# Optimization experiments

Measured on AMD Instinct MI355X. Metric: run time of the kernel, lower is better.

## Reference

```python
import jax, jax.numpy as jnp
import numpy as np

N_NODES = 50000
N_EDGES = 800000
N_GRAPHS = 128
IN_DIM = 100
HID = 256
STEPS = 5


def setup_inputs() -> dict:
    key = jax.random.key(0)
    ks = jax.random.split(key, 24)
    s = 0.05
    inp = {
        'x': jax.random.normal(ks[0], (N_NODES, IN_DIM), jnp.float32),
        'edge_index': jax.random.randint(ks[1], (2, N_EDGES), 0, N_NODES, jnp.int32),
        'batch': jnp.sort(jax.random.randint(ks[2], (N_NODES,), 0, N_GRAPHS, jnp.int32)),
        # input projection
        'W_in': jax.random.normal(ks[3], (IN_DIM, HID), jnp.float32) * s,
        'b_in': jnp.zeros((HID,), jnp.float32),
        # GatedGraphConv per-step weights [steps, HID, HID]
        'ggc_w': jax.random.normal(ks[4], (STEPS, HID, HID), jnp.float32) * s,
        # GRUCell params (torch layout: rows = [r, z, n] chunks)
        'W_ih': jax.random.normal(ks[5], (3 * HID, HID), jnp.float32) * s,
        'W_hh': jax.random.normal(ks[6], (3 * HID, HID), jnp.float32) * s,
        'b_ih': jnp.zeros((3 * HID,), jnp.float32),
        'b_hh': jnp.zeros((3 * HID,), jnp.float32),
        # attention MLP: HID -> HID//2 -> 1 (sigmoid)
        'Wa1': jax.random.normal(ks[7], (HID, HID // 2), jnp.float32) * s,
        'ba1': jnp.zeros((HID // 2,), jnp.float32),
        'Wa2': jax.random.normal(ks[8], (HID // 2, 1), jnp.float32) * s,
        'ba2': jnp.zeros((1,), jnp.float32),
        # classifier: 2*HID -> HID -> HID//2 -> 2
        'Wc1': jax.random.normal(ks[9], (2 * HID, HID), jnp.float32) * s,
        'bc1': jnp.zeros((HID,), jnp.float32),
        'Wc2': jax.random.normal(ks[10], (HID, HID // 2), jnp.float32) * s,
        'bc2': jnp.zeros((HID // 2,), jnp.float32),
        'Wc3': jax.random.normal(ks[11], (HID // 2, 2), jnp.float32) * s,
        'bc3': jnp.zeros((2,), jnp.float32),
    }
    return inp


def _forward(x, edge_index, batch, W_in, b_in, ggc_w, W_ih, W_hh, b_ih, b_hh,
             Wa1, ba1, Wa2, ba2, Wc1, bc1, Wc2, bc2, Wc3, bc3):
    src, dst = edge_index[0], edge_index[1]
    # input projection + relu
    h = jax.nn.relu(x @ W_in + b_in)  # [N, HID]

    def ggc_step(h, w):
        m = h @ w                                   # [N, HID]
        agg = jax.ops.segment_sum(m[src], dst, num_segments=N_NODES)  # scatter-add
        gi = agg @ W_ih.T + b_ih                    # [N, 3*HID]
        gh = h @ W_hh.T + b_hh
        i_r, i_z, i_n = jnp.split(gi, 3, axis=-1)
        h_r, h_z, h_n = jnp.split(gh, 3, axis=-1)
        r = jax.nn.sigmoid(i_r + h_r)
        z = jax.nn.sigmoid(i_z + h_z)
        n = jnp.tanh(i_n + r * h_n)
        return (1.0 - z) * n + z * h, None

    h, _ = jax.lax.scan(ggc_step, h, ggc_w)
    h = jax.nn.relu(h)

    # attention weights per node (dropout is identity at eval)
    a = jax.nn.sigmoid(jax.nn.relu(h @ Wa1 + ba1) @ Wa2 + ba2)[:, 0]  # [N]
    wx = h * a[:, None]

    counts = jax.ops.segment_sum(jnp.ones((N_NODES,), h.dtype), batch, num_segments=N_GRAPHS)
    mean_p = jax.ops.segment_sum(wx, batch, num_segments=N_GRAPHS) / jnp.maximum(counts, 1.0)[:, None]
    max_p = jax.ops.segment_max(wx, batch, num_segments=N_GRAPHS)
    max_p = jnp.where(counts[:, None] > 0, max_p, 0.0)
    g = jnp.concatenate([mean_p, max_p], axis=1)  # [G, 2*HID]

    g = jax.nn.relu(g @ Wc1 + bc1)
    g = jax.nn.relu(g @ Wc2 + bc2)
    preds = g @ Wc3 + bc3
    return preds, a


def reference(x, edge_index, batch, W_in, b_in, ggc_w, W_ih, W_hh, b_ih, b_hh,
              Wa1, ba1, Wa2, ba2, Wc1, bc1, Wc2, bc2, Wc3, bc3):
    return _forward(x, edge_index, batch, W_in, b_in, ggc_w, W_ih, W_hh, b_ih, b_hh,
                    Wa1, ba1, Wa2, ba2, Wc1, bc1, Wc2, bc2, Wc3, bc3)
```

## Files before the change

### kernel.cpp

```cpp
#include <hip/hip_runtime.h>
#include <cstddef>

#define NN 50000
#define NE 800000
#define NG 128
#define IND 100
#define HID 256
#define NSTEPS 5
#define PCH 8

typedef __attribute__((ext_vector_type(8))) short bf16x8;
typedef __attribute__((ext_vector_type(4))) float f32x4;

__device__ __forceinline__ float b2f(unsigned h) { return __uint_as_float(h << 16); }
__device__ __forceinline__ unsigned short f2b(float f) {
    unsigned u = __float_as_uint(f);
    unsigned r = (u + 0x7FFFu + ((u >> 16) & 1u)) >> 16;
    return (unsigned short)r;
}
__device__ __forceinline__ float sigm(float x) { return 1.f / (1.f + __expf(-x)); }
__device__ __forceinline__ float tanh_fast(float x) { return 1.f - 2.f / (1.f + __expf(2.f * x)); }

#define LSTR 40
__global__ __launch_bounds__(256) void gemm_bf16(const unsigned short* __restrict__ A,
                                                 const unsigned short* __restrict__ Bt,
                                                 const float* __restrict__ bias, int act,
                                                 unsigned short* __restrict__ C,
                                                 int M, int N, int K,
                                                 size_t btz, size_t cz)
{
    Bt += (size_t)blockIdx.z * btz;
    C  += (size_t)blockIdx.z * cz;
    __shared__ unsigned short As[128 * LSTR];
    __shared__ unsigned short Bs[128 * LSTR];
    const int tid  = threadIdx.x;
    const int row0 = blockIdx.y * 128;
    const int col0 = blockIdx.x * 128;
    const int wave = tid >> 6, lane = tid & 63;
    const int wm = wave >> 1, wn = wave & 1;
    const int lr = lane & 15, q = lane >> 4;
    const int r_st = tid >> 2;
    const int ks   = tid & 3;

    f32x4 acc[4][4];
    #pragma unroll
    for (int i = 0; i < 4; ++i)
        #pragma unroll
        for (int j = 0; j < 4; ++j) acc[i][j] = (f32x4){0.f, 0.f, 0.f, 0.f};

    for (int k0 = 0; k0 < K; k0 += 32) {
        #pragma unroll
        for (int it = 0; it < 2; ++it) {
            int r  = r_st + it * 64;
            int ga = min(row0 + r, M - 1);
            uint4 av = *(const uint4*)(A + (size_t)ga * K + k0 + ks * 8);
            *(uint4*)(As + r * LSTR + ks * 8) = av;
            uint4 bv = *(const uint4*)(Bt + (size_t)(col0 + r) * K + k0 + ks * 8);
            *(uint4*)(Bs + r * LSTR + ks * 8) = bv;
        }
        __syncthreads();
        bf16x8 af[4], bfr[4];
        #pragma unroll
        for (int i = 0; i < 4; ++i)
            af[i]  = *(const bf16x8*)(As + (wm * 64 + i * 16 + lr) * LSTR + q * 8);
        #pragma unroll
        for (int j = 0; j < 4; ++j)
            bfr[j] = *(const bf16x8*)(Bs + (wn * 64 + j * 16 + lr) * LSTR + q * 8);
        #pragma unroll
        for (int i = 0; i < 4; ++i)
            #pragma unroll
            for (int j = 0; j < 4; ++j)
                acc[i][j] = __builtin_amdgcn_mfma_f32_16x16x32_bf16(af[i], bfr[j], acc[i][j], 0, 0, 0);
        __syncthreads();
    }
    #pragma unroll
    for (int i = 0; i < 4; ++i) {
        int rbase = row0 + wm * 64 + i * 16 + q * 4;
        #pragma unroll
        for (int j = 0; j < 4; ++j) {
            int col = col0 + wn * 64 + j * 16 + lr;
            if (col >= N) continue;
            float badd = bias ? bias[col] : 0.f;
            #pragma unroll
            for (int r = 0; r < 4; ++r) {
                int row = rbase + r;
                if (row < M) {
                    float v = acc[i][j][r] + badd;
                    if (act) v = fmaxf(v, 0.f);
                    C[(size_t)row * N + col] = f2b(v);
                }
            }
        }
    }
}

__global__ __launch_bounds__(256, 3) void gru_mfma(const unsigned short* __restrict__ agg,
                                                   const unsigned short* __restrict__ hbf,
                                                   float* __restrict__ h,
                                                   unsigned short* __restrict__ hbfo,
                                                   const unsigned short* __restrict__ Wgi,
                                                   const unsigned short* __restrict__ Wgh,
                                                   const float* __restrict__ bih,
                                                   const float* __restrict__ bhh,
                                                   int M, int dorelu)
{
    __shared__ unsigned short Sa[64 * LSTR];
    __shared__ unsigned short Sh[64 * LSTR];
    const int tid  = threadIdx.x;
    const int row0 = blockIdx.y * 64;
    const int col0 = blockIdx.x * 64;
    const int wave = tid >> 6, lane = tid & 63;
    const int lr = lane & 15, q = lane >> 4;
    const int cw = col0 + wave * 16;
    const int r_st = tid >> 2, ks = tid & 3;

    f32x4 acc[4][4];
    #pragma unroll
    for (int g = 0; g < 4; ++g)
        #pragma unroll
        for (int i = 0; i < 4; ++i) acc[g][i] = (f32x4){0.f, 0.f, 0.f, 0.f};

    const int ga = min(row0 + r_st, M - 1);
    uint4 pa = *(const uint4*)(agg + (size_t)ga * HID + ks * 8);
    uint4 ph = *(const uint4*)(hbf + (size_t)ga * HID + ks * 8);

    #pragma unroll
    for (int kk = 0; kk < 8; ++kk) {
        const int k0 = kk * 32;
        __syncthreads();
        *(uint4*)(Sa + r_st * LSTR + ks * 8) = pa;
        *(uint4*)(Sh + r_st * LSTR + ks * 8) = ph;
        __syncthreads();
        if (kk < 7) {
            pa = *(const uint4*)(agg + (size_t)ga * HID + k0 + 32 + ks * 8);
            ph = *(const uint4*)(hbf + (size_t)ga * HID + k0 + 32 + ks * 8);
        }
        bf16x8 wir = *(const bf16x8*)(Wgi + (size_t)(0*HID + cw + lr) * HID + k0 + q * 8);
        bf16x8 wiz = *(const bf16x8*)(Wgi + (size_t)(1*HID + cw + lr) * HID + k0 + q * 8);
        bf16x8 win = *(const bf16x8*)(Wgi + (size_t)(2*HID + cw + lr) * HID + k0 + q * 8);
        bf16x8 whr = *(const bf16x8*)(Wgh + (size_t)(0*HID + cw + lr) * HID + k0 + q * 8);
        bf16x8 whz = *(const bf16x8*)(Wgh + (size_t)(1*HID + cw + lr) * HID + k0 + q * 8);
        bf16x8 whn = *(const bf16x8*)(Wgh + (size_t)(2*HID + cw + lr) * HID + k0 + q * 8);
        bf16x8 afa[4], afh[4];
        #pragma unroll
        for (int i = 0; i < 4; ++i) {
            afa[i] = *(const bf16x8*)(Sa + (i * 16 + lr) * LSTR + q * 8);
            afh[i] = *(const bf16x8*)(Sh + (i * 16 + lr) * LSTR + q * 8);
        }
        #pragma unroll
        for (int i = 0; i < 4; ++i) {
            acc[0][i] = __builtin_amdgcn_mfma_f32_16x16x32_bf16(afa[i], wir, acc[0][i], 0, 0, 0);
            acc[0][i] = __builtin_amdgcn_mfma_f32_16x16x32_bf16(afh[i], whr, acc[0][i], 0, 0, 0);
            acc[1][i] = __builtin_amdgcn_mfma_f32_16x16x32_bf16(afa[i], wiz, acc[1][i], 0, 0, 0);
            acc[1][i] = __builtin_amdgcn_mfma_f32_16x16x32_bf16(afh[i], whz, acc[1][i], 0, 0, 0);
            acc[2][i] = __builtin_amdgcn_mfma_f32_16x16x32_bf16(afa[i], win, acc[2][i], 0, 0, 0);
            acc[3][i] = __builtin_amdgcn_mfma_f32_16x16x32_bf16(afh[i], whn, acc[3][i], 0, 0, 0);
        }
    }

    const int cg = cw + lr;
    const float brr = bih[cg]         + bhh[cg];
    const float bzz = bih[HID + cg]   + bhh[HID + cg];
    const float bin = bih[2*HID + cg];
    const float bhn = bhh[2*HID + cg];
    #pragma unroll
    for (int i = 0; i < 4; ++i) {
        #pragma unroll
        for (int r = 0; r < 4; ++r) {
            int row = row0 + i * 16 + q * 4 + r;
            if (row < M) {
                float rr = sigm(acc[0][i][r] + brr);
                float zz = sigm(acc[1][i][r] + bzz);
                float nn = tanh_fast(acc[2][i][r] + bin + rr * (acc[3][i][r] + bhn));
                size_t off = (size_t)row * HID + cg;
                float hv = h[off];
                float o = (1.f - zz) * nn + zz * hv;
                if (dorelu) o = fmaxf(o, 0.f);
                h[off] = o;
                hbfo[off] = f2b(o);
            }
        }
    }
}

template<int ACT>
__global__ __launch_bounds__(256) void gemm_kn(const float* __restrict__ A,
                                               const float* __restrict__ B,
                                               const float* __restrict__ bias,
                                               float* __restrict__ C,
                                               int M, int N, int K)
{
    __shared__ float As[64][17];
    __shared__ float Bs[16][65];
    const int tid  = threadIdx.x;
    const int row0 = blockIdx.y * 64;
    const int col0 = blockIdx.x * 64;
    const int tr = tid >> 4, tc = tid & 15;
    const int ar = tid >> 2, akq = tid & 3;
    const int bk = tid >> 4, bj = (tid & 15) << 2;

    float acc[4][4] = {};
    for (int k0 = 0; k0 < K; k0 += 16) {
        float4 av = make_float4(0.f,0.f,0.f,0.f);
        if (row0 + ar < M && (k0 + (akq<<2)) < K)
            av = *(const float4*)(A + (size_t)(row0+ar)*K + k0 + (akq<<2));
        As[ar][(akq<<2)+0] = av.x; As[ar][(akq<<2)+1] = av.y;
        As[ar][(akq<<2)+2] = av.z; As[ar][(akq<<2)+3] = av.w;
        float4 bv = make_float4(0.f,0.f,0.f,0.f);
        if (k0 + bk < K)
            bv = *(const float4*)(B + (size_t)(k0+bk)*N + col0 + bj);
        Bs[bk][bj+0] = bv.x; Bs[bk][bj+1] = bv.y; Bs[bk][bj+2] = bv.z; Bs[bk][bj+3] = bv.w;
        __syncthreads();
        #pragma unroll
        for (int k = 0; k < 16; ++k) {
            float a4[4], b4[4];
            #pragma unroll
            for (int i = 0; i < 4; ++i) a4[i] = As[(tr<<2)+i][k];
            #pragma unroll
            for (int j = 0; j < 4; ++j) b4[j] = Bs[k][(tc<<2)+j];
            #pragma unroll
            for (int i = 0; i < 4; ++i)
                #pragma unroll
                for (int j = 0; j < 4; ++j) acc[i][j] += a4[i]*b4[j];
        }
        __syncthreads();
    }
    #pragma unroll
    for (int i = 0; i < 4; ++i) {
        int row = row0 + (tr<<2) + i;
        if (row >= M) continue;
        #pragma unroll
        for (int j = 0; j < 4; ++j) {
            int col = col0 + (tc<<2) + j;
            float v = acc[i][j];
            if (bias) v += bias[col];
            if (ACT == 1) v = fmaxf(v, 0.f);
            C[(size_t)row*N + col] = v;
        }
    }
}

__global__ void edge_count(const int* __restrict__ dst, int* __restrict__ cnt, int E) {
    int e = blockIdx.x*256 + threadIdx.x;
    if (e < E) atomicAdd(&cnt[dst[e]], 1);
}
__global__ void scan_bsums(const int* __restrict__ cnt, int* __restrict__ bsum, int n) {
    __shared__ int sd[512];
    int tid = threadIdx.x, i = blockIdx.x*512 + tid;
    sd[tid] = (i < n) ? cnt[i] : 0;
    __syncthreads();
    for (int off = 256; off > 0; off >>= 1) {
        if (tid < off) sd[tid] += sd[tid+off];
        __syncthreads();
    }
    if (tid == 0) bsum[blockIdx.x] = sd[0];
}
__global__ void scan_top(int* __restrict__ bsum, int nb) {
    __shared__ int sd[128];
    int tid = threadIdx.x;
    int v = (tid < nb) ? bsum[tid] : 0;
    sd[tid] = v;
    __syncthreads();
    for (int off = 1; off < 128; off <<= 1) {
        int t = (tid >= off) ? sd[tid-off] : 0;
        __syncthreads();
        sd[tid] += t;
        __syncthreads();
    }
    if (tid < nb) bsum[tid] = sd[tid] - v;
}
__global__ void scan_local(const int* __restrict__ cnt, const int* __restrict__ bsum,
                           int* __restrict__ rp, int n) {
    __shared__ int sd[512];
    int tid = threadIdx.x, i = blockIdx.x*512 + tid;
    int v = (i < n) ? cnt[i] : 0;
    sd[tid] = v;
    __syncthreads();
    for (int off = 1; off < 512; off <<= 1) {
        int t = (tid >= off) ? sd[tid-off] : 0;
        __syncthreads();
        sd[tid] += t;
        __syncthreads();
    }
    if (i < n) rp[i] = bsum[blockIdx.x] + sd[tid] - v;
    if (i == n-1) rp[n] = bsum[blockIdx.x] + sd[tid];
}
__global__ void edge_fill(const int* __restrict__ src, const int* __restrict__ dst,
                          const int* __restrict__ rp, int* __restrict__ cur,
                          int* __restrict__ ci, int E) {
    int e = blockIdx.x*256 + threadIdx.x;
    if (e < E) {
        int d = dst[e];
        int pos = rp[d] + atomicAdd(&cur[d], 1);
        ci[pos] = src[e];
    }
}

__global__ void gather_agg(const unsigned short* __restrict__ m, unsigned short* __restrict__ agg,
                           const int* __restrict__ rp, const int* __restrict__ ci, int M)
{
    int node = blockIdx.x*4 + (threadIdx.x >> 6);
    int lane = threadIdx.x & 63;
    if (node >= M) return;
    const int half = lane >> 5;
    const int li   = lane & 31;
    int s = rp[node], e = rp[node+1];
    float a[8] = {0.f,0.f,0.f,0.f,0.f,0.f,0.f,0.f};
    int p = s;
    for (; p + 7 < e; p += 8) {
        int r0 = ci[p + half], r1 = ci[p + 2 + half], r2 = ci[p + 4 + half], r3 = ci[p + 6 + half];
        uint4 v0 = *(const uint4*)(m + (size_t)r0 * HID + li * 8);
        uint4 v1 = *(const uint4*)(m + (size_t)r1 * HID + li * 8);
        uint4 v2 = *(const uint4*)(m + (size_t)r2 * HID + li * 8);
        uint4 v3 = *(const uint4*)(m + (size_t)r3 * HID + li * 8);
        a[0] += b2f(v0.x & 0xffffu) + b2f(v1.x & 0xffffu) + b2f(v2.x & 0xffffu) + b2f(v3.x & 0xffffu);
        a[1] += b2f(v0.x >> 16)     + b2f(v1.x >> 16)     + b2f(v2.x >> 16)     + b2f(v3.x >> 16);
        a[2] += b2f(v0.y & 0xffffu) + b2f(v1.y & 0xffffu) + b2f(v2.y & 0xffffu) + b2f(v3.y & 0xffffu);
        a[3] += b2f(v0.y >> 16)     + b2f(v1.y >> 16)     + b2f(v2.y >> 16)     + b2f(v3.y >> 16);
        a[4] += b2f(v0.z & 0xffffu) + b2f(v1.z & 0xffffu) + b2f(v2.z & 0xffffu) + b2f(v3.z & 0xffffu);
        a[5] += b2f(v0.z >> 16)     + b2f(v1.z >> 16)     + b2f(v2.z >> 16)     + b2f(v3.z >> 16);
        a[6] += b2f(v0.w & 0xffffu) + b2f(v1.w & 0xffffu) + b2f(v2.w & 0xffffu) + b2f(v3.w & 0xffffu);
        a[7] += b2f(v0.w >> 16)     + b2f(v1.w >> 16)     + b2f(v2.w >> 16)     + b2f(v3.w >> 16);
    }
    for (; p + 1 < e; p += 2) {
        int r0 = ci[p + half];
        uint4 v = *(const uint4*)(m + (size_t)r0 * HID + li * 8);
        a[0] += b2f(v.x & 0xffffu); a[1] += b2f(v.x >> 16);
        a[2] += b2f(v.y & 0xffffu); a[3] += b2f(v.y >> 16);
        a[4] += b2f(v.z & 0xffffu); a[5] += b2f(v.z >> 16);
        a[6] += b2f(v.w & 0xffffu); a[7] += b2f(v.w >> 16);
    }
    if (p < e && half == 0) {
        int r0 = ci[p];
        uint4 v = *(const uint4*)(m + (size_t)r0 * HID + li * 8);
        a[0] += b2f(v.x & 0xffffu); a[1] += b2f(v.x >> 16);
        a[2] += b2f(v.y & 0xffffu); a[3] += b2f(v.y >> 16);
        a[4] += b2f(v.z & 0xffffu); a[5] += b2f(v.z >> 16);
        a[6] += b2f(v.w & 0xffffu); a[7] += b2f(v.w >> 16);
    }
    #pragma unroll
    for (int u = 0; u < 8; ++u) a[u] += __shfl_xor(a[u], 32, 64);
    if (half == 0) {
        uint4 o;
        o.x = (unsigned)f2b(a[0]) | ((unsigned)f2b(a[1]) << 16);
        o.y = (unsigned)f2b(a[2]) | ((unsigned)f2b(a[3]) << 16);
        o.z = (unsigned)f2b(a[4]) | ((unsigned)f2b(a[5]) << 16);
        o.w = (unsigned)f2b(a[6]) | ((unsigned)f2b(a[7]) << 16);
        *(uint4*)(agg + (size_t)node * HID + li * 8) = o;
    }
}

__global__ void cvt_f2b4(const float* __restrict__ src, unsigned short* __restrict__ dst, int n4) {
    int i = blockIdx.x*256 + threadIdx.x;
    if (i >= n4) return;
    float4 v = *((const float4*)src + i);
    uint2 o;
    o.x = (unsigned)f2b(v.x) | ((unsigned)f2b(v.y) << 16);
    o.y = (unsigned)f2b(v.z) | ((unsigned)f2b(v.w) << 16);
    *((uint2*)dst + i) = o;
}
__global__ void cvt_elem(const float* __restrict__ src, unsigned short* __restrict__ dst, int n) {
    int i = blockIdx.x*256 + threadIdx.x;
    if (i < n) dst[i] = f2b(src[i]);
}
__global__ void prep_wa1(const float* __restrict__ w, unsigned short* __restrict__ wt) {
    int n = blockIdx.x, k = threadIdx.x;
    wt[(size_t)n*HID + k] = f2b(w[(size_t)k*128 + n]);
}

__global__ void att_sig(const unsigned short* __restrict__ t, const float* __restrict__ Wa2,
                        const float* __restrict__ ba2, float* __restrict__ a, int M)
{
    int node = blockIdx.x*4 + (threadIdx.x >> 6);
    int lane = threadIdx.x & 63;
    if (node >= M) return;
    float s = b2f(t[(size_t)node*128 + lane])*Wa2[lane]
            + b2f(t[(size_t)node*128 + 64 + lane])*Wa2[64+lane];
    #pragma unroll
    for (int off = 32; off > 0; off >>= 1) s += __shfl_down(s, off, 64);
    if (lane == 0) a[node] = 1.f/(1.f+__expf(-(s + ba2[0])));
}

__device__ __forceinline__ int lowerb(const int* arr, int n, int val) {
    int lo = 0, hi = n;
    while (lo < hi) { int mid = (lo+hi)>>1; if (arr[mid] < val) lo = mid+1; else hi = mid; }
    return lo;
}
__global__ void pool_partial(const float* __restrict__ h, const float* __restrict__ a,
                             const int* __restrict__ batch, float* __restrict__ part, int M)
{
    int g = blockIdx.x, c = blockIdx.y, j = threadIdx.x;
    int lo = lowerb(batch, M, g);
    int hi = lowerb(batch, M, g+1);
    int len = hi - lo, per = (len + PCH - 1) / PCH;
    int s = lo + c * per, e = min(s + per, hi);
    float sum = 0.f, mx = 0.f;
    for (int n = s; n < e; ++n) {
        float v = h[(size_t)n*HID + j] * a[n];
        sum += v; mx = fmaxf(mx, v);
    }
    float* pp = part + ((size_t)g*PCH + c) * 512;
    pp[j] = sum; pp[256 + j] = mx;
}
__global__ void pool_final(const float* __restrict__ part, const int* __restrict__ batch,
                           float* __restrict__ gout, int M)
{
    int g = blockIdx.x, j = threadIdx.x;
    float sum = 0.f, mx = 0.f;
    for (int c = 0; c < PCH; ++c) {
        const float* pp = part + ((size_t)g*PCH + c) * 512;
        sum += pp[j];
        mx = fmaxf(mx, pp[256 + j]);
    }
    int lo = lowerb(batch, M, g);
    int hi = lowerb(batch, M, g+1);
    float cnt = (float)(hi - lo);
    gout[(size_t)g*512 + j]       = sum / fmaxf(cnt, 1.f);
    gout[(size_t)g*512 + 256 + j] = mx;
}

__global__ void preds_kernel(const float* __restrict__ g2, const float* __restrict__ W,
                             const float* __restrict__ b, float* __restrict__ out)
{
    int t = threadIdx.x;
    int row = t >> 1, col = t & 1;
    float s = b[col];
    for (int k = 0; k < 128; ++k) s += g2[row*128 + k] * W[k*2 + col];
    out[row*2 + col] = s;
}

extern "C" void kernel_launch(void* const* d_in, const int* in_sizes, int n_in,
                              void* d_out, int out_size, void* d_ws, size_t ws_size,
                              hipStream_t stream)
{
    const float* x     = (const float*)d_in[0];
    const int*   eidx  = (const int*)  d_in[1];
    const int*   batch = (const int*)  d_in[2];
    const float* W_in  = (const float*)d_in[3];
    const float* b_in  = (const float*)d_in[4];
    const float* ggc_w = (const float*)d_in[5];
    const float* W_ih  = (const float*)d_in[6];
    const float* W_hh  = (const float*)d_in[7];
    const float* b_ih  = (const float*)d_in[8];
    const float* b_hh  = (const float*)d_in[9];
    const float* Wa1   = (const float*)d_in[10];
    const float* ba1   = (const float*)d_in[11];
    const float* Wa2   = (const float*)d_in[12];
    const float* ba2   = (const float*)d_in[13];
    const float* Wc1   = (const float*)d_in[14];
    const float* bc1   = (const float*)d_in[15];
    const float* Wc2   = (const float*)d_in[16];
    const float* bc2   = (const float*)d_in[17];
    const float* Wc3   = (const float*)d_in[18];
    const float* bc3   = (const float*)d_in[19];

    float* out  = (float*)d_out;
    float* aout = out + NG*2;

    char* p = (char*)d_ws;
    auto alloc = [&](size_t bytes) -> char* {
        char* r = p; p += (bytes + 255) & ~(size_t)255; return r;
    };
    float*          hf    = (float*)alloc((size_t)NN*HID*4);
    unsigned short* hbfP  = (unsigned short*)alloc((size_t)NN*HID*2);
    unsigned short* hbfQ  = (unsigned short*)alloc((size_t)NN*HID*2);
    unsigned short* aggbf = (unsigned short*)alloc((size_t)NN*HID*2);
    int* row_ptr = (int*)alloc((NN+1)*4);
    int* cursor  = (int*)alloc(NN*4);
    int* col_idx = (int*)alloc((size_t)NE*4);
    int* bsum    = (int*)alloc(128*4);
    unsigned short* wgbf   = (unsigned short*)alloc((size_t)NSTEPS*HID*HID*2);
    unsigned short* WihBf  = (unsigned short*)alloc((size_t)768*HID*2);
    unsigned short* WhhBf  = (unsigned short*)alloc((size_t)768*HID*2);
    unsigned short* WcombT = (unsigned short*)alloc((size_t)NSTEPS*768*HID*2);
    unsigned short* Wa1t   = (unsigned short*)alloc((size_t)128*HID*2);
    float* part = (float*)alloc((size_t)NG*PCH*512*4);
    float* gbuf = (float*)alloc((size_t)NG*2*HID*4);
    float* g1   = (float*)alloc((size_t)NG*HID*4);
    float* g2   = (float*)alloc((size_t)NG*128*4);

    const int* esrc = eidx;
    const int* edst = eidx + NE;
    dim3 blk(256);
    const int NB512 = (NN + 511) / 512;

    hipMemsetAsync(cursor, 0, NN*sizeof(int), stream);
    edge_count<<<NE/256, blk, 0, stream>>>(edst, cursor, NE);
    scan_bsums<<<NB512, 512, 0, stream>>>(cursor, bsum, NN);
    scan_top<<<1, 128, 0, stream>>>(bsum, NB512);
    scan_local<<<NB512, 512, 0, stream>>>(cursor, bsum, row_ptr, NN);
    hipMemsetAsync(cursor, 0, NN*sizeof(int), stream);
    edge_fill<<<NE/256, blk, 0, stream>>>(esrc, edst, row_ptr, cursor, col_idx, NE);

    cvt_elem<<<(NSTEPS*HID*HID + 255)/256, blk, 0, stream>>>(ggc_w, wgbf, NSTEPS*HID*HID);
    cvt_elem<<<768, blk, 0, stream>>>(W_ih, WihBf, 768*HID);
    cvt_elem<<<768, blk, 0, stream>>>(W_hh, WhhBf, 768*HID);
    prep_wa1<<<128, blk, 0, stream>>>(Wa1, Wa1t);
    gemm_bf16<<<dim3(2, 6, NSTEPS), blk, 0, stream>>>(
        WihBf, wgbf, nullptr, 0, WcombT, 768, HID, HID,
        (size_t)HID*HID, (size_t)768*HID);

    gemm_kn<1><<<dim3(HID/64, (NN+63)/64), blk, 0, stream>>>(x, W_in, b_in, hf, NN, HID, IND);
    cvt_f2b4<<<(NN*HID/4 + 255)/256, blk, 0, stream>>>(hf, hbfP, NN*HID/4);

    unsigned short* hbf  = hbfP;
    unsigned short* hbfn = hbfQ;
    const int MB64 = (NN + 63) / 64;
    for (int s = 0; s < NSTEPS; ++s) {
        gather_agg<<<NN/4, blk, 0, stream>>>(hbf, aggbf, row_ptr, col_idx, NN);
        gru_mfma<<<dim3(HID/64, MB64), blk, 0, stream>>>(
            aggbf, hbf, hf, hbfn, WcombT + (size_t)s*768*HID, WhhBf, b_ih, b_hh,
            NN, (s == NSTEPS-1) ? 1 : 0);
        unsigned short* t0 = hbf; hbf = hbfn; hbfn = t0;
    }

    unsigned short* tbuf = aggbf;
    gemm_bf16<<<dim3(1, (NN+127)/128), blk, 0, stream>>>(hbf, Wa1t, ba1, 1, tbuf, NN, 128, HID, 0, 0);
    att_sig<<<NN/4, blk, 0, stream>>>(tbuf, Wa2, ba2, aout, NN);

    pool_partial<<<dim3(NG, PCH), blk, 0, stream>>>(hf, aout, batch, part, NN);
    pool_final<<<NG, blk, 0, stream>>>(part, batch, gbuf, NN);

    gemm_kn<1><<<dim3(HID/64, (NG+63)/64), blk, 0, stream>>>(gbuf, Wc1, bc1, g1, NG, HID, 2*HID);
    gemm_kn<1><<<dim3(2,      (NG+63)/64), blk, 0, stream>>>(g1,   Wc2, bc2, g2, NG, 128, HID);
    preds_kernel<<<1, blk, 0, stream>>>(g2, Wc3, bc3, out);
}
```

Measured before the change: 1.246 ms.

## Run input projection on bf16 MFMA with hi/lo split of x, raise GRU occupancy

Replaces the fp32 input-projection GEMM and the separate fp32-to-bf16 conversion with a bf16 MFMA GEMM. x is split into hi and lo bf16 parts concatenated along K, and W_in is duplicated to match, which keeps some extra precision. The GEMM writes both the bf16 and fp32 outputs, so the conversion kernel is removed. The GRU kernel's launch bounds are also raised to 4 blocks per CU, which may cause register spills. W_in itself is rounded to bf16, which lowers the precision of the projection.

Result: no change. 1.225 ms (-1.7%).

```diff
diff --git a/kernel.cpp b/kernel.cpp
--- a/kernel.cpp
+++ b/kernel.cpp
@@ -26,6 +26,7 @@
                                                  const unsigned short* __restrict__ Bt,
                                                  const float* __restrict__ bias, int act,
                                                  unsigned short* __restrict__ C,
+                                                 float* __restrict__ Cf,
                                                  int M, int N, int K,
                                                  size_t btz, size_t cz)
 {
@@ -88,13 +89,14 @@
                     float v = acc[i][j][r] + badd;
                     if (act) v = fmaxf(v, 0.f);
                     C[(size_t)row * N + col] = f2b(v);
+                    if (Cf) Cf[(size_t)row * N + col] = v;
                 }
             }
         }
     }
 }
 
-__global__ __launch_bounds__(256, 3) void gru_mfma(const unsigned short* __restrict__ agg,
+__global__ __launch_bounds__(256, 4) void gru_mfma(const unsigned short* __restrict__ agg,
                                                    const unsigned short* __restrict__ hbf,
                                                    float* __restrict__ h,
                                                    unsigned short* __restrict__ hbfo,
@@ -350,15 +352,24 @@
     }
 }
 
-__global__ void cvt_f2b4(const float* __restrict__ src, unsigned short* __restrict__ dst, int n4) {
-    int i = blockIdx.x*256 + threadIdx.x;
-    if (i >= n4) return;
-    float4 v = *((const float4*)src + i);
-    uint2 o;
-    o.x = (unsigned)f2b(v.x) | ((unsigned)f2b(v.y) << 16);
-    o.y = (unsigned)f2b(v.z) | ((unsigned)f2b(v.w) << 16);
-    *((uint2*)dst + i) = o;
-}
+__global__ void split_x(const float* __restrict__ x, unsigned short* __restrict__ A) {
+    int n = blockIdx.x, k = threadIdx.x;
+    unsigned short hi = 0, lo = 0;
+    if (k < IND) {
+        float v = x[(size_t)n * IND + k];
+        hi = f2b(v);
+        lo = f2b(v - b2f(hi));
+    }
+    A[(size_t)n * 256 + k]       = hi;
+    A[(size_t)n * 256 + 128 + k] = lo;
+}
+__global__ void prep_win(const float* __restrict__ w, unsigned short* __restrict__ bt) {
+    int n = blockIdx.x, k = threadIdx.x;
+    unsigned short v = (k < IND) ? f2b(w[(size_t)k * HID + n]) : (unsigned short)0;
+    bt[(size_t)n * 256 + k]       = v;
+    bt[(size_t)n * 256 + 128 + k] = v;
+}
+
 __global__ void cvt_elem(const float* __restrict__ src, unsigned short* __restrict__ dst, int n) {
     int i = blockIdx.x*256 + threadIdx.x;
     if (i < n) dst[i] = f2b(src[i]);
@@ -474,6 +485,7 @@
     unsigned short* WhhBf  = (unsigned short*)alloc((size_t)768*HID*2);
     unsigned short* WcombT = (unsigned short*)alloc((size_t)NSTEPS*768*HID*2);
     unsigned short* Wa1t   = (unsigned short*)alloc((size_t)128*HID*2);
+    unsigned short* WinT   = (unsigned short*)alloc((size_t)256*256*2);
     float* part = (float*)alloc((size_t)NG*PCH*512*4);
     float* gbuf = (float*)alloc((size_t)NG*2*HID*4);
     float* g1   = (float*)alloc((size_t)NG*HID*4);
@@ -497,11 +509,14 @@
     cvt_elem<<<768, blk, 0, stream>>>(W_hh, WhhBf, 768*HID);
     prep_wa1<<<128, blk, 0, stream>>>(Wa1, Wa1t);
     gemm_bf16<<<dim3(2, 6, NSTEPS), blk, 0, stream>>>(
-        WihBf, wgbf, nullptr, 0, WcombT, 768, HID, HID,
+        WihBf, wgbf, nullptr, 0, WcombT, nullptr, 768, HID, HID,
         (size_t)HID*HID, (size_t)768*HID);
 
-    gemm_kn<1><<<dim3(HID/64, (NN+63)/64), blk, 0, stream>>>(x, W_in, b_in, hf, NN, HID, IND);
-    cvt_f2b4<<<(NN*HID/4 + 255)/256, blk, 0, stream>>>(hf, hbfP, NN*HID/4);
+    unsigned short* Ax = hbfQ;
+    split_x<<<NN, 128, 0, stream>>>(x, Ax);
+    prep_win<<<256, 128, 0, stream>>>(W_in, WinT);
+    gemm_bf16<<<dim3(2, (NN+127)/128), blk, 0, stream>>>(
+        Ax, WinT, b_in, 1, hbfP, hf, NN, HID, 256, 0, 0);
 
     unsigned short* hbf  = hbfP;
     unsigned short* hbfn = hbfQ;
@@ -515,7 +530,7 @@
     }
 
     unsigned short* tbuf = aggbf;
-    gemm_bf16<<<dim3(1, (NN+127)/128), blk, 0, stream>>>(hbf, Wa1t, ba1, 1, tbuf, NN, 128, HID, 0, 0);
+    gemm_bf16<<<dim3(1, (NN+127)/128), blk, 0, stream>>>(hbf, Wa1t, ba1, 1, tbuf, nullptr, NN, 128, HID, 0, 0);
     att_sig<<<NN/4, blk, 0, stream>>>(tbuf, Wa2, ba2, aout, NN);
 
     pool_partial<<<dim3(NG, PCH), blk, 0, stream>>>(hf, aout, batch, part, NN);
```
